# Kernel optimization log

Hardware: AMD Instinct MI355X
Metric: run time of the kernel (lower is better)

## Reference

```python
import jax, jax.numpy as jnp
import numpy as np

N_HEADS = 16
D_HEAD = 64
D_MODEL = 1024


def setup_inputs() -> dict:
    key = jax.random.key(0)
    k_x, k_q, k_k, k_v, k_o = jax.random.split(key, 5)
    std = 1.0 / np.sqrt(D_MODEL)
    B, T = 4, 2048
    return {
        "x": jax.random.normal(k_x, (B, T, D_MODEL), dtype=jnp.float32),
        "W_Q": jax.random.normal(k_q, (D_MODEL, N_HEADS * D_HEAD), dtype=jnp.float32) * std,
        "W_K": jax.random.normal(k_k, (D_MODEL, N_HEADS * D_HEAD), dtype=jnp.float32) * std,
        "W_V": jax.random.normal(k_v, (D_MODEL, N_HEADS * D_HEAD), dtype=jnp.float32) * std,
        "W_O": jax.random.normal(k_o, (N_HEADS * D_HEAD, D_MODEL), dtype=jnp.float32) * std,
    }


def reference(x, W_Q, W_K, W_V, W_O):
    B, T, _ = x.shape
    H, D = N_HEADS, D_HEAD
    # projections: [B,T,H,D]
    q = (x @ W_Q).reshape(B, T, H, D)
    k = (x @ W_K).reshape(B, T, H, D)
    v = (x @ W_V).reshape(B, T, H, D)
    scale = 1.0 / jnp.sqrt(jnp.asarray(D, dtype=x.dtype))
    # scores: [B,H,T,T]
    scores = jnp.einsum("bqhd,bkhd->bhqk", q, k) * scale
    causal = jnp.tril(jnp.ones((T, T), dtype=bool))
    scores = jnp.where(causal[None, None], scores, jnp.asarray(-jnp.inf, dtype=scores.dtype))
    attn = jax.nn.softmax(scores, axis=-1)
    out = jnp.einsum("bhqk,bkhd->bqhd", attn, v).reshape(B, T, H * D)
    return out @ W_O
```

## Files before the change

kernel.cpp:

```cpp
#include <hip/hip_runtime.h>

typedef unsigned short u16;
typedef short bf16x8 __attribute__((ext_vector_type(8)));
typedef float f32x4 __attribute__((ext_vector_type(4)));

__device__ inline u16 f32_to_bf16(float f) {
  union { float f; unsigned int u; } v; v.f = f;
  unsigned int r = v.u + 0x7FFFu + ((v.u >> 16) & 1u);
  return (u16)(r >> 16);
}

__device__ inline float red16_sum(float x) {
#pragma unroll
  for (int m = 8; m >= 1; m >>= 1) x += __shfl_xor(x, m);
  return x;
}

__device__ __forceinline__ void gl_lds16(const u16* g, u16* l) {
  __builtin_amdgcn_global_load_lds(
      (const __attribute__((address_space(1))) void*)g,
      (__attribute__((address_space(3))) void*)l, 16, 0, 0);
}

__global__ __launch_bounds__(256) void xcvt_kernel(const float* __restrict__ in,
                                                   u16* __restrict__ out) {
  size_t i = (size_t)blockIdx.x * 256 + threadIdx.x;
  float4 f0 = ((const float4*)in)[2 * i];
  float4 f1 = ((const float4*)in)[2 * i + 1];
  union { u16 t[8]; uint4 v; } pk;
  pk.t[0] = f32_to_bf16(f0.x); pk.t[1] = f32_to_bf16(f0.y);
  pk.t[2] = f32_to_bf16(f0.z); pk.t[3] = f32_to_bf16(f0.w);
  pk.t[4] = f32_to_bf16(f1.x); pk.t[5] = f32_to_bf16(f1.y);
  pk.t[6] = f32_to_bf16(f1.z); pk.t[7] = f32_to_bf16(f1.w);
  ((uint4*)out)[i] = pk.v;
}

__global__ __launch_bounds__(256) void transpose_cvt4_kernel(const float* __restrict__ i0,
                                                             const float* __restrict__ i1,
                                                             const float* __restrict__ i2,
                                                             const float* __restrict__ i3,
                                                             u16* __restrict__ wbase) {
  const int z = blockIdx.z;
  const float* in = (z == 0) ? i0 : (z == 1) ? i1 : (z == 2) ? i2 : i3;
  u16* out = wbase + (size_t)z * (1 << 20);
  __shared__ __align__(16) float tile[32][33];
  const int tx = threadIdx.x & 31, ty = threadIdx.x >> 5;
  const int bx = blockIdx.x * 32, by = blockIdx.y * 32;
#pragma unroll
  for (int i = 0; i < 32; i += 8)
    tile[ty + i][tx] = in[(size_t)(by + ty + i) * 1024 + bx + tx];
  __syncthreads();
#pragma unroll
  for (int i = 0; i < 32; i += 8)
    out[(size_t)(bx + ty + i) * 1024 + by + tx] = f32_to_bf16(tile[tx][ty + i]);
}


#define QKV_BAR asm volatile("s_barrier" ::: "memory")
#define QKV_VMW(n) asm volatile("s_waitcnt vmcnt(" #n ")" ::: "memory")
#define QKV_LGK0 asm volatile("s_waitcnt lgkmcnt(0)" ::: "memory")
#define SCHED0 __builtin_amdgcn_sched_barrier(0)

#define DSR(dst, addr, off) \
  asm volatile("ds_read_b128 %0, %1 offset:" #off : "=v"(dst) : "v"(addr))

#define LDA_ALL(ad) { DSR(afr[0], ad, 0);    DSR(afr[1], ad, 1024); \
                      DSR(afr[2], ad, 2048); DSR(afr[3], ad, 3072); }
#define LDB_ALL(bd) { DSR(bfr[0], bd, 0);    DSR(bfr[1], bd, 1024); \
                      DSR(bfr[2], bd, 2048); DSR(bfr[3], bd, 3072); }

#define STAGE_A(d2, kh, kt)                                        \
    gl_lds16(A + aSrc + (size_t)(kt) * 64 + (kh) * 32,             \
             &sA[d2][kh][wave * 512])
#define STAGE_B(d2, kh, kt) do {                                   \
    const u16* _p = Bt + bSrc + (size_t)(kt) * 64 + (kh) * 32;     \
    gl_lds16(_p, &sB[d2][kh][wave * 1024]);                        \
    gl_lds16(_p + 16 * 1024, &sB[d2][kh][wave * 1024 + 512]);      \
  } while (0)
#define MMA4 {                                                     \
    _Pragma("unroll") for (int mt = 0; mt < 4; ++mt)               \
      _Pragma("unroll") for (int nt = 0; nt < 4; ++nt)             \
        acc[mt][nt] = __builtin_amdgcn_mfma_f32_16x16x32_bf16(     \
            afr[mt], bfr[nt], acc[mt][nt], 0, 0, 0); }

__global__ __launch_bounds__(512, 2) void gemm_qkv_kernel(const u16* __restrict__ A,
                                                          const u16* __restrict__ Bt,
                                                          u16* __restrict__ Q,
                                                          u16* __restrict__ K,
                                                          u16* __restrict__ Vt) {
  __shared__ __align__(16) u16 sA[2][2][128 * 32];
  __shared__ __align__(16) u16 sB[2][2][256 * 32];

  const int tid = threadIdx.x;
  const int lane = tid & 63, wave = tid >> 6;
  const int quad = lane >> 4, l16 = lane & 15;

  const int lin = blockIdx.y * 12 + blockIdx.x;
  const int swz = (lin & 7) * 96 + (lin >> 3);
  const int bn = swz % 12, bm = swz / 12;
  const int m0 = bm * 128, n0 = bn * 256;
  const int wm = (wave >> 2) * 64, wn = (wave & 3) * 64;

  const int sRow = lane >> 2;
  const int sGrp = (lane & 3) ^ ((lane >> 3) & 3);
  const size_t aSrc = (size_t)(m0 + wave * 16 + sRow) * 1024 + sGrp * 8;
  const size_t bSrc = (size_t)(n0 + wave * 32 + sRow) * 1024 + sGrp * 8;

  const int swr = (quad ^ ((l16 >> 1) & 3)) * 8;
  const unsigned aRd = (unsigned)(size_t)&sA[0][0][0] +
                       (unsigned)(((wm + l16) * 32 + swr) * 2);
  const unsigned bRd = (unsigned)(size_t)&sB[0][0][0] +
                       (unsigned)(((wn + l16) * 32 + swr) * 2);

  f32x4 acc[4][4] = {};
  bf16x8 afr[4], bfr[4];

  STAGE_A(0, 0, 0); STAGE_B(0, 0, 0); STAGE_A(0, 1, 0); STAGE_B(0, 1, 0);
  QKV_VMW(0);
  QKV_BAR;

  for (int t = 0; t < 16; ++t) {
    const int d = t & 1, dn = d ^ 1;
    const bool pf = (t < 15);
    const unsigned a0 = aRd + (unsigned)(d * 16384);
    const unsigned b0 = bRd + (unsigned)(d * 32768);

    if (pf) { STAGE_A(dn, 0, t + 1); STAGE_B(dn, 0, t + 1); }
    LDB_ALL(b0); LDA_ALL(a0);
    QKV_LGK0;
    SCHED0;
    __builtin_amdgcn_s_setprio(1);
    MMA4;
    __builtin_amdgcn_s_setprio(0);
    SCHED0;

    if (pf) { STAGE_A(dn, 1, t + 1); STAGE_B(dn, 1, t + 1); }
    LDB_ALL(b0 + 16384u); LDA_ALL(a0 + 8192u);
    QKV_LGK0;
    SCHED0;
    __builtin_amdgcn_s_setprio(1);
    MMA4;
    __builtin_amdgcn_s_setprio(0);
    SCHED0;

    QKV_VMW(0);
    QKV_BAR;
  }

  const int proj = bn >> 2;
#pragma unroll
  for (int mt = 0; mt < 4; ++mt) {
#pragma unroll
    for (int nt = 0; nt < 4; ++nt) {
#pragma unroll
      for (int r = 0; r < 4; ++r) {
        int mrow = m0 + wm + mt * 16 + quad * 4 + r;
        int nloc = (n0 & 1023) + wn + nt * 16 + l16;
        u16 bv = f32_to_bf16(acc[mt][nt][r]);
        if (proj == 0) {
          Q[(size_t)mrow * 1024 + nloc] = bv;
        } else if (proj == 1) {
          K[(size_t)mrow * 1024 + nloc] = bv;
        } else {
          int b = mrow >> 11, tt = mrow & 2047;
          int h = nloc >> 6, dd = nloc & 63;
          Vt[((size_t)((b * 16 + h) * 64 + dd)) * 2048 + tt] = bv;
        }
      }
    }
  }
}

#undef STAGE_A
#undef STAGE_B
#undef MMA4
#undef LDA_ALL
#undef LDB_ALL


#define LDA_ALL(ad) { DSR(afr[0], ad, 0);    DSR(afr[1], ad, 1024); \
                      DSR(afr[2], ad, 2048); DSR(afr[3], ad, 3072); }
#define LDB_ALL(bd) { DSR(bfr[0], bd, 0);    DSR(bfr[1], bd, 1024); \
                      DSR(bfr[2], bd, 2048); DSR(bfr[3], bd, 3072); }
#define OSTAGE_A(d2, kh, kt)                                            \
    gl_lds16(A + aSrc + (size_t)(kt) * 64 + (kh) * 32,                  \
             &sA[d2][kh][wave * 512])
#define OSTAGE_B(d2, kh, kt) do {                                       \
    const u16* _p = Bt + bSrc + (size_t)(kt) * 64 + (kh) * 32;          \
    gl_lds16(_p, &sB[d2][kh][wave * 1024]);                             \
    gl_lds16(_p + 16 * 1024, &sB[d2][kh][wave * 1024 + 512]);           \
  } while (0)
#define OMMA {                                                          \
    _Pragma("unroll") for (int mt = 0; mt < 4; ++mt)                    \
      _Pragma("unroll") for (int nt = 0; nt < 4; ++nt)                  \
        acc[mt][nt] = __builtin_amdgcn_mfma_f32_16x16x32_bf16(          \
            afr[mt], bfr[nt], acc[mt][nt], 0, 0, 0); }

__global__ __launch_bounds__(512, 2) void gemm_out_kernel(const u16* __restrict__ A,
                                                          const u16* __restrict__ Bt,
                                                          float* __restrict__ C) {
  __shared__ __align__(16) u16 sA[2][2][128 * 32];
  __shared__ __align__(16) u16 sB[2][2][256 * 32];

  const int tid = threadIdx.x;
  const int lane = tid & 63, wave = tid >> 6;
  const int quad = lane >> 4, l16 = lane & 15;

  const int lin = blockIdx.y * 4 + blockIdx.x;
  const int swz = (lin & 7) * 32 + (lin >> 3);
  const int bn = swz & 3, bm = swz >> 2;
  const int m0 = bm * 128, n0 = bn * 256;
  const int wm = (wave >> 2) * 64, wn = (wave & 3) * 64;

  const int sRow = lane >> 2;
  const int sGrp = (lane & 3) ^ ((lane >> 3) & 3);
  const size_t aSrc = (size_t)(m0 + wave * 16 + sRow) * 1024 + sGrp * 8;
  const size_t bSrc = (size_t)(n0 + wave * 32 + sRow) * 1024 + sGrp * 8;

  const int swr = (quad ^ ((l16 >> 1) & 3)) * 8;
  const unsigned aRd = (unsigned)(size_t)&sA[0][0][0] +
                       (unsigned)(((wm + l16) * 32 + swr) * 2);
  const unsigned bRd = (unsigned)(size_t)&sB[0][0][0] +
                       (unsigned)(((wn + l16) * 32 + swr) * 2);

  f32x4 acc[4][4] = {};
  bf16x8 afr[4], bfr[4];

  OSTAGE_A(0, 0, 0); OSTAGE_B(0, 0, 0); OSTAGE_A(0, 1, 0); OSTAGE_B(0, 1, 0);
  QKV_VMW(0);
  QKV_BAR;

  for (int t = 0; t < 16; ++t) {
    const int d = t & 1, dn = d ^ 1;
    const bool pf = (t < 15);
    const unsigned a0 = aRd + (unsigned)(d * 16384);
    const unsigned b0 = bRd + (unsigned)(d * 32768);

    if (pf) { OSTAGE_A(dn, 0, t + 1); OSTAGE_B(dn, 0, t + 1); }
    LDB_ALL(b0); LDA_ALL(a0);
    QKV_LGK0;
    SCHED0;
    __builtin_amdgcn_s_setprio(1);
    OMMA;
    __builtin_amdgcn_s_setprio(0);
    SCHED0;

    if (pf) { OSTAGE_A(dn, 1, t + 1); OSTAGE_B(dn, 1, t + 1); }
    LDB_ALL(b0 + 16384u); LDA_ALL(a0 + 8192u);
    QKV_LGK0;
    SCHED0;
    __builtin_amdgcn_s_setprio(1);
    OMMA;
    __builtin_amdgcn_s_setprio(0);
    SCHED0;

    QKV_VMW(0);
    QKV_BAR;
  }

#pragma unroll
  for (int mt = 0; mt < 4; ++mt)
#pragma unroll
    for (int nt = 0; nt < 4; ++nt)
#pragma unroll
      for (int r = 0; r < 4; ++r) {
        int mrow = m0 + wm + mt * 16 + quad * 4 + r;
        int ncol = n0 + wn + nt * 16 + l16;
        C[(size_t)mrow * 1024 + ncol] = acc[mt][nt][r];
      }
}

#undef OSTAGE_A
#undef OSTAGE_B
#undef LDA_ALL
#undef LDB_ALL
#undef OMMA

#define LDS_S 72

__global__ __launch_bounds__(256, 4) void attn_kernel(const u16* __restrict__ Qm,
                                                      const u16* __restrict__ Km,
                                                      const u16* __restrict__ Vt,
                                                      u16* __restrict__ Ctx) {
  const int pi = blockIdx.x;
  const int h = blockIdx.y, b = blockIdx.z;
  const int tid = threadIdx.x, lane = tid & 63, wave = tid >> 6;
  const int quad = lane >> 4, l16 = lane & 15;
  const int q64[2] = {pi, 31 - pi};

  __shared__ __align__(16) u16 sK[64 * LDS_S];
  __shared__ __align__(16) u16 sV[64 * LDS_S];
  __shared__ __align__(16) u16 sP[4][2][16 * LDS_S];

  bf16x8 qf[2][2];
#pragma unroll
  for (int s = 0; s < 2; ++s) {
    const size_t qrow = (size_t)(b * 2048 + q64[s] * 64 + wave * 16 + l16);
#pragma unroll
    for (int kk = 0; kk < 2; ++kk)
      qf[s][kk] = *(const bf16x8*)(Qm + qrow * 1024 + h * 64 + kk * 32 + quad * 8);
  }

  f32x4 o_acc[2][4] = {};
  float ps[2][4] = {};

  const int nkt = 32 - pi;
  for (int kt = 0; kt < nkt; ++kt) {
    const int k0 = kt * 64;
    __syncthreads();
#pragma unroll
    for (int i = 0; i < 2; ++i) {
      int c = tid + 256 * i;
      int row = c >> 3, col = (c & 7) * 8;
      *(uint4*)(sK + row * LDS_S + col) =
          *(const uint4*)(Km + ((size_t)(b * 2048 + k0 + row)) * 1024 + h * 64 + col);
      *(uint4*)(sV + row * LDS_S + col) =
          *(const uint4*)(Vt + ((size_t)((b * 16 + h) * 64 + row)) * 2048 + k0 + col);
    }
    __syncthreads();

#pragma unroll
    for (int s = 0; s < 2; ++s) {
      const int qmin = q64[s] * 64 + wave * 16;
      if (k0 > qmin + 15) continue;

      f32x4 sc[4];
#pragma unroll
      for (int nt = 0; nt < 4; ++nt) {
        f32x4 a = {};
#pragma unroll
        for (int kk = 0; kk < 2; ++kk) {
          bf16x8 kf = *(const bf16x8*)(sK + (nt * 16 + l16) * LDS_S + kk * 32 + quad * 8);
          a = __builtin_amdgcn_mfma_f32_16x16x32_bf16(qf[s][kk], kf, a, 0, 0, 0);
        }
        sc[nt] = a;
      }

      const bool need_mask = (k0 + 63) > qmin;
#pragma unroll
      for (int nt = 0; nt < 4; ++nt) {
#pragma unroll
        for (int r = 0; r < 4; ++r) {
          float v = sc[nt][r] * 0.125f;
          if (need_mask) {
            int qi = qmin + quad * 4 + r;
            int kj = k0 + nt * 16 + l16;
            if (kj > qi) v = -1e30f;
          }
          float p = __expf(v);
          sc[nt][r] = p;
          ps[s][r] += p;
        }
      }

#pragma unroll
      for (int nt = 0; nt < 4; ++nt)
#pragma unroll
        for (int r = 0; r < 4; ++r)
          sP[wave][s][(quad * 4 + r) * LDS_S + nt * 16 + l16] = f32_to_bf16(sc[nt][r]);

#pragma unroll
      for (int kk = 0; kk < 2; ++kk) {
        bf16x8 pf = *(const bf16x8*)(sP[wave][s] + l16 * LDS_S + kk * 32 + quad * 8);
#pragma unroll
        for (int dt = 0; dt < 4; ++dt) {
          bf16x8 vf = *(const bf16x8*)(sV + (dt * 16 + l16) * LDS_S + kk * 32 + quad * 8);
          o_acc[s][dt] = __builtin_amdgcn_mfma_f32_16x16x32_bf16(pf, vf,
                                                                 o_acc[s][dt], 0, 0, 0);
        }
      }
    }
  }

  float inv_l[2][4];
#pragma unroll
  for (int s = 0; s < 2; ++s)
#pragma unroll
    for (int r = 0; r < 4; ++r)
      inv_l[s][r] = 1.0f / red16_sum(ps[s][r]);

#pragma unroll
  for (int s = 0; s < 2; ++s)
#pragma unroll
    for (int dt = 0; dt < 4; ++dt)
#pragma unroll
      for (int r = 0; r < 4; ++r) {
        int trow = q64[s] * 64 + wave * 16 + quad * 4 + r;
        Ctx[((size_t)(b * 2048 + trow)) * 1024 + h * 64 + dt * 16 + l16] =
            f32_to_bf16(o_acc[s][dt][r] * inv_l[s][r]);
      }
}

extern "C" void kernel_launch(void* const* d_in, const int* in_sizes, int n_in,
                              void* d_out, int out_size, void* d_ws, size_t ws_size,
                              hipStream_t stream) {
  const float* x  = (const float*)d_in[0];
  const float* wq = (const float*)d_in[1];
  const float* wk = (const float*)d_in[2];
  const float* wv = (const float*)d_in[3];
  const float* wo = (const float*)d_in[4];
  u16* ws = (u16*)d_ws;

  u16* wtqkv = ws;
  u16* wto  = ws + 3 * (size_t)(1 << 20);
  u16* Q    = ws + 4 * (size_t)(1 << 20);
  u16* K    = ws + 12 * (size_t)(1 << 20);
  u16* Vt   = ws + 20 * (size_t)(1 << 20);
  u16* Ctx  = ws + 28 * (size_t)(1 << 20);
  u16* xb   = Ctx;
  float* out = (float*)d_out;

  dim3 tb(256);
  xcvt_kernel<<<dim3(4096), tb, 0, stream>>>(x, xb);
  transpose_cvt4_kernel<<<dim3(32, 32, 4), tb, 0, stream>>>(wq, wk, wv, wo, ws);

  gemm_qkv_kernel<<<dim3(12, 64), dim3(512), 0, stream>>>(xb, wtqkv, Q, K, Vt);

  attn_kernel<<<dim3(16, 16, 4), tb, 0, stream>>>(Q, K, Vt, Ctx);

  gemm_out_kernel<<<dim3(4, 64), dim3(512), 0, stream>>>(Ctx, wto, out);
}
```

Measured before the change: 296.5 us.

## Enlarge QKV GEMM tile to 256x256 with 1024-thread blocks

Rebuilds the QKV projection GEMM around a 256x256 output tile computed by 16 waves per block, instead of a 128x256 tile with 8 waves. Each pipeline stage now loads one 32-wide K slice for A and B, giving 32 single-MMA-batch iterations in place of 16 double-batch ones. The grid is halved and the block swizzle adjusted to match. This raises operand reuse per block and cuts redundant global loads of B. In exchange it doubles the number of barrier rounds, now synchronising 1024 threads, and leaves fewer, larger blocks to balance across the CUs.

```diff
diff --git a/kernel.cpp b/kernel.cpp
--- a/kernel.cpp
+++ b/kernel.cpp
@@ -69,77 +69,62 @@
 #define LDB_ALL(bd) { DSR(bfr[0], bd, 0);    DSR(bfr[1], bd, 1024); \
                       DSR(bfr[2], bd, 2048); DSR(bfr[3], bd, 3072); }
 
-#define STAGE_A(d2, kh, kt)                                        \
-    gl_lds16(A + aSrc + (size_t)(kt) * 64 + (kh) * 32,             \
-             &sA[d2][kh][wave * 512])
-#define STAGE_B(d2, kh, kt) do {                                   \
-    const u16* _p = Bt + bSrc + (size_t)(kt) * 64 + (kh) * 32;     \
-    gl_lds16(_p, &sB[d2][kh][wave * 1024]);                        \
-    gl_lds16(_p + 16 * 1024, &sB[d2][kh][wave * 1024 + 512]);      \
-  } while (0)
-#define MMA4 {                                                     \
+#define QSTAGE_A(p, kh) gl_lds16(A + aSrc + (size_t)(kh) * 32, &sA[p][wave * 512])
+#define QSTAGE_B(p, kh) gl_lds16(Bt + bSrc + (size_t)(kh) * 32, &sB[p][wave * 512])
+#define MMA16 {                                                    \
     _Pragma("unroll") for (int mt = 0; mt < 4; ++mt)               \
       _Pragma("unroll") for (int nt = 0; nt < 4; ++nt)             \
         acc[mt][nt] = __builtin_amdgcn_mfma_f32_16x16x32_bf16(     \
             afr[mt], bfr[nt], acc[mt][nt], 0, 0, 0); }
 
-__global__ __launch_bounds__(512, 2) void gemm_qkv_kernel(const u16* __restrict__ A,
-                                                          const u16* __restrict__ Bt,
-                                                          u16* __restrict__ Q,
-                                                          u16* __restrict__ K,
-                                                          u16* __restrict__ Vt) {
-  __shared__ __align__(16) u16 sA[2][2][128 * 32];
-  __shared__ __align__(16) u16 sB[2][2][256 * 32];
+__global__ __launch_bounds__(1024, 4) void gemm_qkv_kernel(const u16* __restrict__ A,
+                                                           const u16* __restrict__ Bt,
+                                                           u16* __restrict__ Q,
+                                                           u16* __restrict__ K,
+                                                           u16* __restrict__ Vt) {
+  __shared__ __align__(16) u16 sA[2][256 * 32];
+  __shared__ __align__(16) u16 sB[2][256 * 32];
 
   const int tid = threadIdx.x;
   const int lane = tid & 63, wave = tid >> 6;
   const int quad = lane >> 4, l16 = lane & 15;
 
   const int lin = blockIdx.y * 12 + blockIdx.x;
-  const int swz = (lin & 7) * 96 + (lin >> 3);
+  const int swz = (lin & 7) * 48 + (lin >> 3);
   const int bn = swz % 12, bm = swz / 12;
-  const int m0 = bm * 128, n0 = bn * 256;
+  const int m0 = bm * 256, n0 = bn * 256;
   const int wm = (wave >> 2) * 64, wn = (wave & 3) * 64;
 
-  const int sRow = lane >> 2;
-  const int sGrp = (lane & 3) ^ ((lane >> 3) & 3);
-  const size_t aSrc = (size_t)(m0 + wave * 16 + sRow) * 1024 + sGrp * 8;
-  const size_t bSrc = (size_t)(n0 + wave * 32 + sRow) * 1024 + sGrp * 8;
+  const int srow = tid >> 2;
+  const int sgrp = (tid & 3) ^ ((tid >> 3) & 3);
+  const size_t aSrc = (size_t)(m0 + srow) * 1024 + sgrp * 8;
+  const size_t bSrc = (size_t)(n0 + srow) * 1024 + sgrp * 8;
 
   const int swr = (quad ^ ((l16 >> 1) & 3)) * 8;
-  const unsigned aRd = (unsigned)(size_t)&sA[0][0][0] +
+  const unsigned aRd = (unsigned)(size_t)&sA[0][0] +
                        (unsigned)(((wm + l16) * 32 + swr) * 2);
-  const unsigned bRd = (unsigned)(size_t)&sB[0][0][0] +
+  const unsigned bRd = (unsigned)(size_t)&sB[0][0] +
                        (unsigned)(((wn + l16) * 32 + swr) * 2);
 
   f32x4 acc[4][4] = {};
   bf16x8 afr[4], bfr[4];
 
-  STAGE_A(0, 0, 0); STAGE_B(0, 0, 0); STAGE_A(0, 1, 0); STAGE_B(0, 1, 0);
+  QSTAGE_A(0, 0); QSTAGE_B(0, 0);
   QKV_VMW(0);
   QKV_BAR;
 
-  for (int t = 0; t < 16; ++t) {
-    const int d = t & 1, dn = d ^ 1;
-    const bool pf = (t < 15);
-    const unsigned a0 = aRd + (unsigned)(d * 16384);
-    const unsigned b0 = bRd + (unsigned)(d * 32768);
-
-    if (pf) { STAGE_A(dn, 0, t + 1); STAGE_B(dn, 0, t + 1); }
+  for (int kh = 0; kh < 32; ++kh) {
+    const int p = kh & 1, pn = p ^ 1;
+    const bool pf = (kh < 31);
+    const unsigned a0 = aRd + (unsigned)(p * 16384);
+    const unsigned b0 = bRd + (unsigned)(p * 16384);
+
+    if (pf) { QSTAGE_A(pn, kh + 1); QSTAGE_B(pn, kh + 1); }
     LDB_ALL(b0); LDA_ALL(a0);
     QKV_LGK0;
     SCHED0;
     __builtin_amdgcn_s_setprio(1);
-    MMA4;
-    __builtin_amdgcn_s_setprio(0);
-    SCHED0;
-
-    if (pf) { STAGE_A(dn, 1, t + 1); STAGE_B(dn, 1, t + 1); }
-    LDB_ALL(b0 + 16384u); LDA_ALL(a0 + 8192u);
-    QKV_LGK0;
-    SCHED0;
-    __builtin_amdgcn_s_setprio(1);
-    MMA4;
+    MMA16;
     __builtin_amdgcn_s_setprio(0);
     SCHED0;
 
@@ -171,17 +156,11 @@
   }
 }
 
-#undef STAGE_A
-#undef STAGE_B
-#undef MMA4
-#undef LDA_ALL
-#undef LDB_ALL
-
-
-#define LDA_ALL(ad) { DSR(afr[0], ad, 0);    DSR(afr[1], ad, 1024); \
-                      DSR(afr[2], ad, 2048); DSR(afr[3], ad, 3072); }
-#define LDB_ALL(bd) { DSR(bfr[0], bd, 0);    DSR(bfr[1], bd, 1024); \
-                      DSR(bfr[2], bd, 2048); DSR(bfr[3], bd, 3072); }
+#undef QSTAGE_A
+#undef QSTAGE_B
+#undef MMA16
+
+
 #define OSTAGE_A(d2, kh, kt)                                            \
     gl_lds16(A + aSrc + (size_t)(kt) * 64 + (kh) * 32,                  \
              &sA[d2][kh][wave * 512])
@@ -272,8 +251,6 @@
 
 #undef OSTAGE_A
 #undef OSTAGE_B
-#undef LDA_ALL
-#undef LDB_ALL
 #undef OMMA
 
 #define LDS_S 72
@@ -414,7 +391,7 @@
   xcvt_kernel<<<dim3(4096), tb, 0, stream>>>(x, xb);
   transpose_cvt4_kernel<<<dim3(32, 32, 4), tb, 0, stream>>>(wq, wk, wv, wo, ws);
 
-  gemm_qkv_kernel<<<dim3(12, 64), dim3(512), 0, stream>>>(xb, wtqkv, Q, K, Vt);
+  gemm_qkv_kernel<<<dim3(12, 32), dim3(1024), 0, stream>>>(xb, wtqkv, Q, K, Vt);
 
   attn_kernel<<<dim3(16, 16, 4), tb, 0, stream>>>(Q, K, Vt, Ctx);
 
```

Result: faster. 285.3 us (-3.8%).
